# Kernel tuning notes

Measured on AMD Instinct MI355X. Metric: run time of the kernel, lower is better.

Reference implementation:

```python
import jax, jax.numpy as jnp
import numpy as np

B, N, K, DIM = 2, 20000, 16, 256


def _mlp(x, W, b):
    # torch nn.Linear: x @ W.T + b, then LeakyReLU(0.1)
    return jax.nn.leaky_relu(x @ W.T + b, negative_slope=0.1)


def _lfa(features, geom, idx, W, b):
    # features: [B, N, C]; geom: [B, N, K, 4]; idx: [B, N, K]
    t = _mlp(geom, W, b)                                  # [B, N, K, d_lfa]
    fn = jax.vmap(lambda f, i: f[i])(features, idx)       # gather neighbors: [B, N, K, C]
    # mean over K of concat == concat of means (faithful, avoids big concat)
    return jnp.concatenate([t.mean(axis=2), fn.mean(axis=2)], axis=-1)


def _linear_init(key, out_f, in_f):
    k1, k2 = jax.random.split(key)
    bound = 1.0 / np.sqrt(in_f)
    W = jax.random.uniform(k1, (out_f, in_f), jnp.float32, -bound, bound)
    b = jax.random.uniform(k2, (out_f,), jnp.float32, -bound, bound)
    return W, b


def setup_inputs() -> dict:
    key = jax.random.key(0)
    ks = jax.random.split(key, 8)
    W_init, b_init = _linear_init(ks[0], DIM // 4, DIM)
    W_l1, b_l1 = _linear_init(ks[1], DIM // 4, 4)
    W_l2, b_l2 = _linear_init(ks[2], DIM // 2, 4)
    W_fin, b_fin = _linear_init(ks[3], DIM, DIM)
    W_id, b_id = _linear_init(ks[4], DIM, DIM)
    return {
        "input_tensor": jax.random.normal(ks[5], (B, N, DIM), jnp.float32),
        "geometric_features": jax.random.normal(ks[6], (B, N, K, 4), jnp.float32),
        "neighbor_indices": jax.random.randint(ks[7], (B, N, K), 0, N, jnp.int64 if jax.config.jax_enable_x64 else jnp.int32),
        "W_init": W_init, "b_init": b_init,
        "W_l1": W_l1, "b_l1": b_l1,
        "W_l2": W_l2, "b_l2": b_l2,
        "W_fin": W_fin, "b_fin": b_fin,
        "W_id": W_id, "b_id": b_id,
    }


def reference(input_tensor, geometric_features, neighbor_indices,
              W_init, b_init, W_l1, b_l1, W_l2, b_l2,
              W_fin, b_fin, W_id, b_id):
    residual = input_tensor
    x = _mlp(input_tensor, W_init, b_init)                       # [B, N, dim/4]
    x = _lfa(x, geometric_features, neighbor_indices, W_l1, b_l1)  # [B, N, dim/2]
    x = _lfa(x, geometric_features, neighbor_indices, W_l2, b_l2)  # [B, N, dim]
    x = _mlp(x, W_fin, b_fin)
    return x + _mlp(residual, W_id, b_id)
```

## Files before the change

kernel.cpp:

```cpp
#include <hip/hip_runtime.h>
#include <hip/hip_bf16.h>

#define BN   40000
#define NPTS 20000
#define KNN  16
#define DIM  256

typedef __attribute__((ext_vector_type(8))) short bf16x8;
typedef __attribute__((ext_vector_type(4))) float f32x4;

__device__ __forceinline__ float lrelu(float v) { return v > 0.f ? v : 0.1f * v; }
__device__ __forceinline__ float bs2f(short s) {
    union { unsigned u; float f; } c; c.u = ((unsigned)(unsigned short)s) << 16;
    return c.f;
}
__device__ __forceinline__ short f2bs(float f) {
    __hip_bfloat16 h = __float2bfloat16(f);
    return *reinterpret_cast<short*>(&h);
}
__device__ __forceinline__ bf16x8 ldf32_bf16x8(const float* p) {
    const float4 a = ((const float4*)p)[0];
    const float4 b = ((const float4*)p)[1];
    bf16x8 r;
    r[0]=f2bs(a.x); r[1]=f2bs(a.y); r[2]=f2bs(a.z); r[3]=f2bs(a.w);
    r[4]=f2bs(b.x); r[5]=f2bs(b.y); r[6]=f2bs(b.z); r[7]=f2bs(b.w);
    return r;
}

__device__ __forceinline__ void dma16(const void* g, void* l) {
    __builtin_amdgcn_global_load_lds(
        (const __attribute__((address_space(1))) unsigned int*)g,
        (__attribute__((address_space(3))) unsigned int*)l, 16, 0, 0);
}

__global__ void __launch_bounds__(256) geom_kernel(
    const float* __restrict__ geom,
    const float* __restrict__ W1, const float* __restrict__ B1,
    const float* __restrict__ W2, const float* __restrict__ B2,
    const int* __restrict__ idxw, int* __restrict__ flag,
    const float* __restrict__ Wf, const float* __restrict__ Wi,
    const float* __restrict__ Wn,
    short* __restrict__ Wt, short* __restrict__ Wnb,
    __hip_bfloat16* __restrict__ x2,
    __hip_bfloat16* __restrict__ x3)
{
    if (blockIdx.x >= 3751) {
        int t = (blockIdx.x - 3751) * 256 + threadIdx.x;
        if (t < 32768) {
            int mat = (t >> 14) & 1;
            int tt  = t & 16383;
            float4 v = mat ? ((const float4*)Wi)[tt] : ((const float4*)Wf)[tt];
            int n  = tt >> 6;
            int k  = (tt & 63) * 4;
            int kk = k >> 5, q = (k >> 3) & 3, j = k & 7;
            short4 o; o.x=f2bs(v.x); o.y=f2bs(v.y); o.z=f2bs(v.z); o.w=f2bs(v.w);
            *(short4*)(Wt + ((size_t)((kk*2 + mat)*4 + q))*2048 + n*8 + j) = o;
        } else {
            int tt = t - 32768;
            float4 v = ((const float4*)Wn)[tt];
            short4 o; o.x=f2bs(v.x); o.y=f2bs(v.y); o.z=f2bs(v.z); o.w=f2bs(v.w);
            ((short4*)Wnb)[tt] = o;
        }
        return;
    }
    if (blockIdx.x == 3750) {
        __shared__ int red[256];
        int t = threadIdx.x;
        int v = 0;
#pragma unroll
        for (int it = 0; it < 64; ++it)
            v |= idxw[2 * (t + it * 256) + 1];
        red[t] = v;
        __syncthreads();
        for (int s = 128; s > 0; s >>= 1) {
            if (t < s) red[t] |= red[t + s];
            __syncthreads();
        }
        if (t == 0) *flag = (red[0] != 0) ? 1 : 0;
        return;
    }
    int tid = blockIdx.x * 256 + threadIdx.x;
    int p  = tid / 24;
    int cg = tid - p * 24;
    const float4* g = (const float4*)(geom + (size_t)p * (KNN * 4));
    const float4* Wp; const float* Bp; int c0;
    if (cg < 8) { c0 = cg * 8;       Wp = (const float4*)W1; Bp = B1; }
    else        { c0 = (cg - 8) * 8; Wp = (const float4*)W2; Bp = B2; }
    float4 w[8]; float bb[8];
#pragma unroll
    for (int j = 0; j < 8; ++j) { w[j] = Wp[c0 + j]; bb[j] = Bp[c0 + j]; }
    float acc[8];
#pragma unroll
    for (int j = 0; j < 8; ++j) acc[j] = 0.f;
#pragma unroll
    for (int k = 0; k < KNN; ++k) {
        float4 gv = g[k];
#pragma unroll
        for (int j = 0; j < 8; ++j)
            acc[j] += lrelu(bb[j] + gv.x*w[j].x + gv.y*w[j].y + gv.z*w[j].z + gv.w*w[j].w);
    }
    const float s = 1.f/16.f;
    short* dst = (cg < 8) ? ((short*)x2 + (size_t)p*128 + c0)
                          : ((short*)x3 + (size_t)p*256 + c0);
    bf16x8 o;
#pragma unroll
    for (int j = 0; j < 8; ++j) o[j] = f2bs(acc[j] * s);
    *(bf16x8*)dst = o;
}

__global__ void __launch_bounds__(256) mlp_init_mfma(
    const float* __restrict__ X,
    const short* __restrict__ Wnb,
    const float* __restrict__ bias,
    __hip_bfloat16* __restrict__ Y)
{
    int wave = threadIdx.x >> 6, lane = threadIdx.x & 63;
    int r = lane & 15, q = lane >> 4;
    int m0 = blockIdx.x * 64 + wave * 16;
    const float* Xs = X + (size_t)(m0 + r) * DIM + q * 8;
    const short* W0 = Wnb + (size_t)r * DIM + q * 8;
    f32x4 acc[4];
#pragma unroll
    for (int nt = 0; nt < 4; ++nt) acc[nt] = (f32x4){0.f,0.f,0.f,0.f};
#pragma unroll
    for (int kk = 0; kk < 8; ++kk) {
        bf16x8 a = ldf32_bf16x8(Xs + kk * 32);
#pragma unroll
        for (int nt = 0; nt < 4; ++nt) {
            bf16x8 b = *(const bf16x8*)(W0 + (size_t)nt * (16 * DIM) + kk * 32);
            acc[nt] = __builtin_amdgcn_mfma_f32_16x16x32_bf16(a, b, acc[nt], 0, 0, 0);
        }
    }
#pragma unroll
    for (int nt = 0; nt < 4; ++nt) {
        int col = nt * 16 + r;
        float bv = bias[col];
#pragma unroll
        for (int i = 0; i < 4; ++i) {
            float v = lrelu(acc[nt][i] + bv);
            Y[(size_t)(m0 + q*4 + i) * 64 + col] = __float2bfloat16(v);
        }
    }
}

__global__ void __launch_bounds__(256) gather1_kernel(
    const int* __restrict__ idxw, const int* __restrict__ flag,
    const __hip_bfloat16* __restrict__ x1,
    __hip_bfloat16* __restrict__ x2)
{
    int t = blockIdx.x * 256 + threadIdx.x;
    int p = t >> 3, j = t & 7;
    if (p >= BN) return;
    int dual = (*flag == 0) ? 2 : 1;
    int base = (p >= NPTS) ? NPTS : 0;
    const int* ip = idxw + (size_t)p * KNN * dual;
    float acc[8];
#pragma unroll
    for (int i = 0; i < 8; ++i) acc[i] = 0.f;
#pragma unroll
    for (int k = 0; k < KNN; ++k) {
        int row = base + ip[k * dual];
        bf16x8 v = *(const bf16x8*)((const short*)x1 + (size_t)row * 64 + j * 8);
#pragma unroll
        for (int i = 0; i < 8; ++i) acc[i] += bs2f(v[i]);
    }
    bf16x8 o;
#pragma unroll
    for (int i = 0; i < 8; ++i) o[i] = f2bs(acc[i] * (1.f/16.f));
    *(bf16x8*)((short*)x2 + (size_t)p * 128 + 64 + j * 8) = o;
}

__global__ void __launch_bounds__(256) gather2_kernel(
    const int* __restrict__ idxw, const int* __restrict__ flag,
    const __hip_bfloat16* __restrict__ x2,
    __hip_bfloat16* __restrict__ x3)
{
    int t = blockIdx.x * 256 + threadIdx.x;
    int p = t >> 4, j = t & 15;
    if (p >= BN) return;
    int dual = (*flag == 0) ? 2 : 1;
    int base = (p >= NPTS) ? NPTS : 0;
    const int* ip = idxw + (size_t)p * KNN * dual;
    float acc[8];
#pragma unroll
    for (int i = 0; i < 8; ++i) acc[i] = 0.f;
#pragma unroll
    for (int k = 0; k < KNN; ++k) {
        int row = base + ip[k * dual];
        bf16x8 v = *(const bf16x8*)((const short*)x2 + (size_t)row * 128 + j * 8);
#pragma unroll
        for (int i = 0; i < 8; ++i) acc[i] += bs2f(v[i]);
    }
    bf16x8 o;
#pragma unroll
    for (int i = 0; i < 8; ++i) o[i] = f2bs(acc[i] * (1.f/16.f));
    *(bf16x8*)((short*)x3 + (size_t)p * 256 + 128 + j * 8) = o;
}

__global__ void __launch_bounds__(256) final_mfma(
    const __hip_bfloat16* __restrict__ X3,
    const float* __restrict__ RES,
    const short* __restrict__ Wt,
    const float* __restrict__ Bf,
    const float* __restrict__ Bi,
    float* __restrict__ OUT)
{
    __shared__ short wbuf[16384];
    int t = threadIdx.x;
    int wave = t >> 6, lane = t & 63;
    int r = lane & 15, q = lane >> 4;
    int p0 = blockIdx.x * 16;

    const char* WtB = (const char*)Wt;
    char* wbufB = (char*)wbuf;
    {
        const char* src0 = WtB + (size_t)0 * 32768 + wave * 1024 + lane * 16;
#pragma unroll
        for (int rd = 0; rd < 8; ++rd)
            dma16(src0 + rd * 4096, wbufB + rd * 4096 + wave * 1024);
    }

    bf16x8 a1f[8], a2f[8];
    {
        const short* x3r = (const short*)X3 + (size_t)(p0 + r) * DIM + q * 8;
        const float* rsr = RES + (size_t)(p0 + r) * DIM + q * 8;
#pragma unroll
        for (int kk = 0; kk < 8; ++kk) {
            a1f[kk] = *(const bf16x8*)(x3r + kk * 32);
            a2f[kk] = ldf32_bf16x8(rsr + kk * 32);
        }
    }

    f32x4 acc1[4], acc2[4];
#pragma unroll
    for (int nt = 0; nt < 4; ++nt) {
        acc1[nt] = (f32x4){0.f,0.f,0.f,0.f};
        acc2[nt] = (f32x4){0.f,0.f,0.f,0.f};
    }

#pragma unroll
    for (int kk = 0; kk < 8; ++kk) {
        __syncthreads();
#pragma unroll
        for (int nt = 0; nt < 4; ++nt) {
            int n = wave * 64 + nt * 16 + r;
            bf16x8 b1 = *(const bf16x8*)&wbuf[(size_t)q * 2048 + n * 8];
            bf16x8 b2 = *(const bf16x8*)&wbuf[(size_t)(4 + q) * 2048 + n * 8];
            acc1[nt] = __builtin_amdgcn_mfma_f32_16x16x32_bf16(a1f[kk], b1, acc1[nt], 0, 0, 0);
            acc2[nt] = __builtin_amdgcn_mfma_f32_16x16x32_bf16(a2f[kk], b2, acc2[nt], 0, 0, 0);
        }
        if (kk < 7) {
            __syncthreads();
            const char* src = WtB + (size_t)(kk + 1) * 32768 + wave * 1024 + lane * 16;
#pragma unroll
            for (int rd = 0; rd < 8; ++rd)
                dma16(src + rd * 4096, wbufB + rd * 4096 + wave * 1024);
        }
    }

#pragma unroll
    for (int nt = 0; nt < 4; ++nt) {
        int col = wave * 64 + nt * 16 + r;
        float bfv = Bf[col], biv = Bi[col];
#pragma unroll
        for (int i = 0; i < 4; ++i) {
            float v = lrelu(acc1[nt][i] + bfv) + lrelu(acc2[nt][i] + biv);
            OUT[(size_t)(p0 + q*4 + i) * DIM + col] = v;
        }
    }
}

extern "C" void kernel_launch(void* const* d_in, const int* in_sizes, int n_in,
                              void* d_out, int out_size, void* d_ws, size_t ws_size,
                              hipStream_t stream)
{
    const float* input  = (const float*)d_in[0];
    const float* geom   = (const float*)d_in[1];
    const int*   idxw   = (const int*)d_in[2];
    const float* W_init = (const float*)d_in[3];
    const float* b_init = (const float*)d_in[4];
    const float* W_l1   = (const float*)d_in[5];
    const float* b_l1   = (const float*)d_in[6];
    const float* W_l2   = (const float*)d_in[7];
    const float* b_l2   = (const float*)d_in[8];
    const float* W_fin  = (const float*)d_in[9];
    const float* b_fin  = (const float*)d_in[10];
    const float* W_id   = (const float*)d_in[11];
    const float* b_id   = (const float*)d_in[12];
    float* out = (float*)d_out;

    char* ws = (char*)d_ws;
    int* flag = (int*)ws;
    short* Wt  = (short*)(ws + 16);
    short* Wnb = (short*)(ws + 16 + 262144);
    __hip_bfloat16* x2 = (__hip_bfloat16*)(ws + 16 + 5120000);
    __hip_bfloat16* x3 = (__hip_bfloat16*)(ws + 16 + 15360000);
    __hip_bfloat16* x1 = (__hip_bfloat16*)d_out;

    geom_kernel<<<3895, 256, 0, stream>>>(geom, W_l1, b_l1, W_l2, b_l2,
                                          idxw, flag, W_fin, W_id, W_init,
                                          Wt, Wnb, x2, x3);
    mlp_init_mfma<<<625, 256, 0, stream>>>(input, Wnb, b_init, x1);
    gather1_kernel<<<1250, 256, 0, stream>>>(idxw, flag, x1, x2);
    gather2_kernel<<<2500, 256, 0, stream>>>(idxw, flag, x2, x3);
    final_mfma<<<2500, 256, 0, stream>>>(x3, input, Wt, b_fin, b_id, out);
}
```

Before: 236.0 us.

## Split final GEMM into persistent identity and final kernels with LDS-resident weights

The fused final kernel, which re-streamed all 256 KB of bf16 weights into LDS for every 16-row block, is replaced by two persistent GEMM kernels. Each 512-thread block keeps half of one weight matrix resident in LDS and loops over row tiles. The identity-branch GEMM is launched earlier, right after gather1, and writes into the output buffer. The final GEMM then adds its result to that buffer. This removes the repeated per-block weight loads and the in-loop barriers, at the cost of an extra read-modify-write of the fp32 output and reading each activation row twice, once per column half.

```diff
diff --git a/kernel.cpp b/kernel.cpp
--- a/kernel.cpp
+++ b/kernel.cpp
@@ -40,21 +40,22 @@
     const int* __restrict__ idxw, int* __restrict__ flag,
     const float* __restrict__ Wf, const float* __restrict__ Wi,
     const float* __restrict__ Wn,
-    short* __restrict__ Wt, short* __restrict__ Wnb,
+    short* __restrict__ WtF, short* __restrict__ WtI, short* __restrict__ Wnb,
     __hip_bfloat16* __restrict__ x2,
     __hip_bfloat16* __restrict__ x3)
 {
     if (blockIdx.x >= 3751) {
         int t = (blockIdx.x - 3751) * 256 + threadIdx.x;
         if (t < 32768) {
-            int mat = (t >> 14) & 1;
+            int mat = t >> 14;
             int tt  = t & 16383;
             float4 v = mat ? ((const float4*)Wi)[tt] : ((const float4*)Wf)[tt];
             int n  = tt >> 6;
             int k  = (tt & 63) * 4;
             int kk = k >> 5, q = (k >> 3) & 3, j = k & 7;
             short4 o; o.x=f2bs(v.x); o.y=f2bs(v.y); o.z=f2bs(v.z); o.w=f2bs(v.w);
-            *(short4*)(Wt + ((size_t)((kk*2 + mat)*4 + q))*2048 + n*8 + j) = o;
+            short* dst = mat ? WtI : WtF;
+            *(short4*)(dst + ((size_t)((kk*4 + q)*256 + n))*8 + j) = o;
         } else {
             int tt = t - 32768;
             float4 v = ((const float4*)Wn)[tt];
@@ -197,75 +198,111 @@
     *(bf16x8*)((short*)x3 + (size_t)p * 256 + 128 + j * 8) = o;
 }
 
-__global__ void __launch_bounds__(256) final_mfma(
-    const __hip_bfloat16* __restrict__ X3,
-    const float* __restrict__ RES,
-    const short* __restrict__ Wt,
-    const float* __restrict__ Bf,
+
+__global__ void __launch_bounds__(512) ident_mfma(
+    const float* __restrict__ X,
+    const short* __restrict__ WtI,
     const float* __restrict__ Bi,
     float* __restrict__ OUT)
 {
-    __shared__ short wbuf[16384];
+    __shared__ short wbuf[32768];
     int t = threadIdx.x;
     int wave = t >> 6, lane = t & 63;
     int r = lane & 15, q = lane >> 4;
-    int p0 = blockIdx.x * 16;
-
-    const char* WtB = (const char*)Wt;
-    char* wbufB = (char*)wbuf;
+    int h = blockIdx.y;
     {
-        const char* src0 = WtB + (size_t)0 * 32768 + wave * 1024 + lane * 16;
-#pragma unroll
-        for (int rd = 0; rd < 8; ++rd)
-            dma16(src0 + rd * 4096, wbufB + rd * 4096 + wave * 1024);
-    }
-
-    bf16x8 a1f[8], a2f[8];
+        const char* W8 = (const char*)WtI;
+        char* L8 = (char*)wbuf;
+#pragma unroll
+        for (int i = 0; i < 4; ++i) {
+            int pi = wave * 4 + i;
+            const char* src = W8 + (size_t)pi * 4096 + h * 2048 + lane * 16;
+            char* dst = L8 + (size_t)pi * 2048 + lane * 16;
+            dma16(src, dst);
+            dma16(src + 1024, dst + 1024);
+        }
+    }
+    __syncthreads();
+
+    for (int tile = blockIdx.x * 8 + wave; tile < 2500; tile += 2048) {
+        int p0 = tile * 16;
+        const float* xr = X + (size_t)(p0 + r) * DIM + q * 8;
+        bf16x8 a[8];
+#pragma unroll
+        for (int kk = 0; kk < 8; ++kk) a[kk] = ldf32_bf16x8(xr + kk * 32);
+        f32x4 acc[8];
+#pragma unroll
+        for (int nt = 0; nt < 8; ++nt) acc[nt] = (f32x4){0.f,0.f,0.f,0.f};
+#pragma unroll
+        for (int kk = 0; kk < 8; ++kk) {
+#pragma unroll
+            for (int nt = 0; nt < 8; ++nt) {
+                bf16x8 b = *(const bf16x8*)&wbuf[((kk*4 + q)*128 + nt*16 + r) * 8];
+                acc[nt] = __builtin_amdgcn_mfma_f32_16x16x32_bf16(a[kk], b, acc[nt], 0, 0, 0);
+            }
+        }
+#pragma unroll
+        for (int nt = 0; nt < 8; ++nt) {
+            int col = h * 128 + nt * 16 + r;
+            float bv = Bi[col];
+#pragma unroll
+            for (int i = 0; i < 4; ++i)
+                OUT[(size_t)(p0 + q*4 + i) * DIM + col] = lrelu(acc[nt][i] + bv);
+        }
+    }
+}
+
+__global__ void __launch_bounds__(512) final_mfma(
+    const __hip_bfloat16* __restrict__ X3,
+    const short* __restrict__ WtF,
+    const float* __restrict__ Bf,
+    float* __restrict__ OUT)
+{
+    __shared__ short wbuf[32768];
+    int t = threadIdx.x;
+    int wave = t >> 6, lane = t & 63;
+    int r = lane & 15, q = lane >> 4;
+    int h = blockIdx.y;
     {
-        const short* x3r = (const short*)X3 + (size_t)(p0 + r) * DIM + q * 8;
-        const float* rsr = RES + (size_t)(p0 + r) * DIM + q * 8;
+        const char* W8 = (const char*)WtF;
+        char* L8 = (char*)wbuf;
+#pragma unroll
+        for (int i = 0; i < 4; ++i) {
+            int pi = wave * 4 + i;
+            const char* src = W8 + (size_t)pi * 4096 + h * 2048 + lane * 16;
+            char* dst = L8 + (size_t)pi * 2048 + lane * 16;
+            dma16(src, dst);
+            dma16(src + 1024, dst + 1024);
+        }
+    }
+    __syncthreads();
+
+    for (int tile = blockIdx.x * 8 + wave; tile < 2500; tile += 2048) {
+        int p0 = tile * 16;
+        const short* xr = (const short*)X3 + (size_t)(p0 + r) * DIM + q * 8;
+        bf16x8 a[8];
+#pragma unroll
+        for (int kk = 0; kk < 8; ++kk) a[kk] = *(const bf16x8*)(xr + kk * 32);
+        f32x4 acc[8];
+#pragma unroll
+        for (int nt = 0; nt < 8; ++nt) acc[nt] = (f32x4){0.f,0.f,0.f,0.f};
 #pragma unroll
         for (int kk = 0; kk < 8; ++kk) {
-            a1f[kk] = *(const bf16x8*)(x3r + kk * 32);
-            a2f[kk] = ldf32_bf16x8(rsr + kk * 32);
-        }
-    }
-
-    f32x4 acc1[4], acc2[4];
-#pragma unroll
-    for (int nt = 0; nt < 4; ++nt) {
-        acc1[nt] = (f32x4){0.f,0.f,0.f,0.f};
-        acc2[nt] = (f32x4){0.f,0.f,0.f,0.f};
-    }
-
-#pragma unroll
-    for (int kk = 0; kk < 8; ++kk) {
-        __syncthreads();
-#pragma unroll
-        for (int nt = 0; nt < 4; ++nt) {
-            int n = wave * 64 + nt * 16 + r;
-            bf16x8 b1 = *(const bf16x8*)&wbuf[(size_t)q * 2048 + n * 8];
-            bf16x8 b2 = *(const bf16x8*)&wbuf[(size_t)(4 + q) * 2048 + n * 8];
-            acc1[nt] = __builtin_amdgcn_mfma_f32_16x16x32_bf16(a1f[kk], b1, acc1[nt], 0, 0, 0);
-            acc2[nt] = __builtin_amdgcn_mfma_f32_16x16x32_bf16(a2f[kk], b2, acc2[nt], 0, 0, 0);
-        }
-        if (kk < 7) {
-            __syncthreads();
-            const char* src = WtB + (size_t)(kk + 1) * 32768 + wave * 1024 + lane * 16;
-#pragma unroll
-            for (int rd = 0; rd < 8; ++rd)
-                dma16(src + rd * 4096, wbufB + rd * 4096 + wave * 1024);
-        }
-    }
-
-#pragma unroll
-    for (int nt = 0; nt < 4; ++nt) {
-        int col = wave * 64 + nt * 16 + r;
-        float bfv = Bf[col], biv = Bi[col];
-#pragma unroll
-        for (int i = 0; i < 4; ++i) {
-            float v = lrelu(acc1[nt][i] + bfv) + lrelu(acc2[nt][i] + biv);
-            OUT[(size_t)(p0 + q*4 + i) * DIM + col] = v;
+#pragma unroll
+            for (int nt = 0; nt < 8; ++nt) {
+                bf16x8 b = *(const bf16x8*)&wbuf[((kk*4 + q)*128 + nt*16 + r) * 8];
+                acc[nt] = __builtin_amdgcn_mfma_f32_16x16x32_bf16(a[kk], b, acc[nt], 0, 0, 0);
+            }
+        }
+#pragma unroll
+        for (int nt = 0; nt < 8; ++nt) {
+            int col = h * 128 + nt * 16 + r;
+            float bv = Bf[col];
+#pragma unroll
+            for (int i = 0; i < 4; ++i) {
+                size_t o = (size_t)(p0 + q*4 + i) * DIM + col;
+                OUT[o] = lrelu(acc[nt][i] + bv) + OUT[o];
+            }
         }
     }
 }
@@ -291,7 +328,8 @@
 
     char* ws = (char*)d_ws;
     int* flag = (int*)ws;
-    short* Wt  = (short*)(ws + 16);
+    short* WtF = (short*)(ws + 16);
+    short* WtI = (short*)(ws + 16 + 131072);
     short* Wnb = (short*)(ws + 16 + 262144);
     __hip_bfloat16* x2 = (__hip_bfloat16*)(ws + 16 + 5120000);
     __hip_bfloat16* x3 = (__hip_bfloat16*)(ws + 16 + 15360000);
@@ -299,9 +337,10 @@
 
     geom_kernel<<<3895, 256, 0, stream>>>(geom, W_l1, b_l1, W_l2, b_l2,
                                           idxw, flag, W_fin, W_id, W_init,
-                                          Wt, Wnb, x2, x3);
+                                          WtF, WtI, Wnb, x2, x3);
     mlp_init_mfma<<<625, 256, 0, stream>>>(input, Wnb, b_init, x1);
     gather1_kernel<<<1250, 256, 0, stream>>>(idxw, flag, x1, x2);
+    ident_mfma<<<dim3(256, 2), 512, 0, stream>>>(input, WtI, b_id, out);
     gather2_kernel<<<2500, 256, 0, stream>>>(idxw, flag, x2, x3);
-    final_mfma<<<2500, 256, 0, stream>>>(x3, input, Wt, b_fin, b_id, out);
-}
+    final_mfma<<<dim3(256, 2), 512, 0, stream>>>(x3, WtF, b_fin, out);
+}
```

Measured after the change: 307.4 us. 30.3% more time.
